# Kernel tuning notes

Measured on AMD Instinct MI355X. Metric: run time of the kernel, lower is better.

The kernel has to match this reference:

```python
import jax, jax.numpy as jnp
import numpy as np

N_COARSE = 64
N_FINE = 64  # n_fine_depth = 0
HIDDEN = 128
R = 16384


def setup_inputs() -> dict:
    key = jax.random.key(0)
    ks = jax.random.split(key, 8)
    origins = jax.random.normal(ks[0], (R, 3), dtype=jnp.float32)
    dirs = jax.random.normal(ks[1], (R, 3), dtype=jnp.float32)
    dirs = dirs / jnp.linalg.norm(dirs, axis=-1, keepdims=True)
    near = jnp.full((R, 1), 2.0, dtype=jnp.float32)
    far = jnp.full((R, 1), 6.0, dtype=jnp.float32)
    rays = jnp.concatenate([origins, dirs, near, far], axis=-1)  # [R, 8]
    u_coarse = jax.random.uniform(ks[2], (R, N_COARSE), dtype=jnp.float32)
    u_fine = jax.random.uniform(ks[3], (R, N_FINE), dtype=jnp.float32)
    u_jitter = jax.random.uniform(ks[4], (R, N_FINE), dtype=jnp.float32)
    W1 = jax.random.normal(ks[5], (3, HIDDEN), dtype=jnp.float32) * 0.5
    b1 = jnp.zeros((HIDDEN,), dtype=jnp.float32)
    W2 = jax.random.normal(ks[6], (HIDDEN, 4), dtype=jnp.float32) * 0.1
    b2 = jnp.zeros((4,), dtype=jnp.float32)
    return dict(rays=rays, u_coarse=u_coarse, u_fine=u_fine, u_jitter=u_jitter,
                W1=W1, b1=b1, W2=W2, b2=b2)


def _mlp(pts, W1, b1, W2, b2):
    # pts: [R, K, 3] -> [R, K, 4] (r, g, b, sigma)
    h = jax.nn.relu(pts @ W1 + b1)
    return h @ W2 + b2


def _composite(rays, z_sample, W1, b1, W2, b2):
    # z_sample: [R, K]; faithful to NeRFRenderer.composite
    deltas = jnp.concatenate(
        [z_sample[:, 1:] - z_sample[:, :-1], rays[:, 7:8] - z_sample[:, -1:]], axis=-1)
    pts = rays[:, None, :3] + z_sample[..., None] * rays[:, None, 3:6]  # [R, K, 3]
    out = _mlp(pts, W1, b1, W2, b2)
    rgbs = out[..., :3]
    sigmas = out[..., 3]
    alphas = 1.0 - jnp.exp(-deltas * jax.nn.relu(sigmas))
    alphas_shifted = jnp.concatenate(
        [jnp.ones_like(alphas[:, :1]), 1.0 - alphas + 1e-10], axis=-1)
    T = jnp.cumprod(alphas_shifted, axis=-1)
    weights = alphas * T[:, :-1]  # [R, K]
    rgb_final = jnp.sum(weights[..., None] * rgbs, axis=-2)  # [R, 3]
    depth_final = jnp.sum(weights * z_sample, axis=-1)       # [R]
    return weights, rgb_final, depth_final


def reference(rays, u_coarse, u_fine, u_jitter, W1, b1, W2, b2):
    near, far = rays[:, 6:7], rays[:, 7:8]
    # ---- coarse stratified sampling ----
    step = 1.0 / N_COARSE
    z_steps = jnp.linspace(0.0, 1.0 - step, N_COARSE, dtype=jnp.float32)[None, :] \
        + u_coarse * step
    z_coarse = near * (1.0 - z_steps) + far * z_steps  # [R, Kc] (lindisp=False)
    w_c, rgb_c, depth_c = _composite(rays, z_coarse, W1, b1, W2, b2)
    # ---- fine importance sampling (inverse CDF on detached coarse weights) ----
    w = jax.lax.stop_gradient(w_c) + 1e-5
    pdf = w / jnp.sum(w, axis=-1, keepdims=True)
    cdf = jnp.cumsum(pdf, axis=-1)
    cdf = jnp.concatenate([jnp.zeros_like(cdf[:, :1]), cdf], axis=-1)  # [R, Kc+1]
    inds = jax.vmap(lambda c, u: jnp.searchsorted(c, u, side='right'))(cdf, u_fine)
    inds = jnp.maximum(inds.astype(jnp.float32) - 1.0, 0.0)
    zf_steps = (inds + u_jitter) / N_COARSE
    z_fine = near * (1.0 - zf_steps) + far * zf_steps  # [R, Kf]
    z_all = jnp.sort(jnp.concatenate([z_coarse, z_fine], axis=-1), axis=-1)  # [R, Kc+Kf]
    w_f, rgb_f, depth_f = _composite(rays, z_all, W1, b1, W2, b2)
    # pack outputs: [R, 8] = [coarse rgb(3), coarse depth(1), fine rgb(3), fine depth(1)]
    return jnp.concatenate(
        [rgb_c, depth_c[:, None], rgb_f, depth_f[:, None]], axis=-1)
```

## Files before the change

### kernel.cpp

```cpp
#include <hip/hip_runtime.h>

#define HID 128

typedef _Float16 f16x8 __attribute__((ext_vector_type(8)));
typedef _Float16 f16x2 __attribute__((ext_vector_type(2)));
typedef float f32x4 __attribute__((ext_vector_type(4)));

union HV { f16x8 v; f16x2 h[4]; };
union F8 { float4 v[2]; float f[8]; };

template <int CTRL, int RM = 0xF, int BM = 0xF>
__device__ __forceinline__ float updf(float old, float src) {
    int o = __builtin_bit_cast(int, old);
    int s = __builtin_bit_cast(int, src);
    int r = __builtin_amdgcn_update_dpp(o, s, CTRL, RM, BM, false);
    return __builtin_bit_cast(float, r);
}

__device__ __forceinline__ float readlanef(float v, int l) {
    return __builtin_bit_cast(float, __builtin_amdgcn_readlane(__builtin_bit_cast(int, v), l));
}

__device__ __forceinline__ float dscan_add(float v) {
    v += updf<0x111>(0.0f, v);
    v += updf<0x112>(0.0f, v);
    v += updf<0x114>(0.0f, v);
    v += updf<0x118>(0.0f, v);
    v += updf<0x142, 0xA>(0.0f, v);
    v += updf<0x143, 0xC>(0.0f, v);
    return v;
}

__device__ __forceinline__ float dscan_mul(float v) {
    v *= updf<0x111>(1.0f, v);
    v *= updf<0x112>(1.0f, v);
    v *= updf<0x114>(1.0f, v);
    v *= updf<0x118>(1.0f, v);
    v *= updf<0x142, 0xA>(1.0f, v);
    v *= updf<0x143, 0xC>(1.0f, v);
    return v;
}

__device__ __forceinline__ float dexcl(float incl, float ident) {
    return updf<0x138>(ident, incl);
}
__device__ __forceinline__ float dnext(float v) {
    return updf<0x130>(0.0f, v);
}

template <int IMM>
__device__ __forceinline__ float swzf(float v) {
    return __builtin_bit_cast(float,
        __builtin_amdgcn_ds_swizzle(__builtin_bit_cast(int, v), IMM));
}

template <int M>
__device__ __forceinline__ float bx(float v) {
    if constexpr (M == 1)       return updf<0xB1>(v, v);
    else if constexpr (M == 2)  return updf<0x4E>(v, v);
    else if constexpr (M == 4)  return swzf<0x101F>(v);
    else if constexpr (M == 8)  return swzf<0x201F>(v);
    else if constexpr (M == 16) return swzf<0x401F>(v);
    else                        return __shfl_xor(v, 32, 64);
}

template <int M>
__device__ __forceinline__ float mstep(float x, int lane) {
    const float o = bx<M>(x);
    return ((lane & M) == 0) ? fminf(x, o) : fmaxf(x, o);
}

__device__ __forceinline__ f16x2 pk2(float a, float b) {
    return f16x2{ (_Float16)a, (_Float16)b };
}

__device__ __forceinline__ f32x4 mlp_tile(float zf,
                                          const HV P[4], const HV Q[4],
                                          const f16x8 w2t[4]) {
    const _Float16 zh = (_Float16)zf;
    const f16x2 zp = { zh, zh };
    const f16x2 zero2 = { (_Float16)0, (_Float16)0 };
    f32x4 C = { 0.0f, 0.0f, 0.0f, 0.0f };
#pragma unroll
    for (int c = 0; c < 4; ++c) {
        HV hb;
#pragma unroll
        for (int r = 0; r < 4; ++r) {
            f16x2 acc = Q[c].h[r] * zp + P[c].h[r];
            hb.h[r] = __builtin_elementwise_max(acc, zero2);
        }
        C = __builtin_amdgcn_mfma_f32_16x16x32_f16(w2t[c], hb.v, C, 0, 0, 0);
    }
    return C;
}

extern "C" __global__ void __launch_bounds__(256)
nerf_fused(const float* __restrict__ rays,
           const float* __restrict__ u_coarse,
           const float* __restrict__ u_fine,
           const float* __restrict__ u_jitter,
           const float* __restrict__ W1,
           const float* __restrict__ b1,
           const float* __restrict__ W2,
           const float* __restrict__ b2,
           float* __restrict__ out) {
    const int lane = threadIdx.x & 63;
    const int wv   = threadIdx.x >> 6;
    const int ray  = (blockIdx.x << 2) + wv;
    const int s16  = lane & 15;
    const int g    = lane >> 4;

    __shared__ float s_cdf[4][65];
    __shared__ float s_zc [4][64];
    __shared__ float s_za [4][128];

    const float* rp = rays + ray * 8;
    const float ox = rp[0], oy = rp[1], oz = rp[2];
    const float dx = rp[3], dy = rp[4], dz = rp[5];
    const float nearv = rp[6], farv = rp[7];

    HV P[4], Q[4];
#pragma unroll
    for (int c = 0; c < 4; ++c) {
        const int hid0 = 32 * c + 8 * g;
        F8 wa, wb, wc, bb;
        wa.v[0] = *(const float4*)(W1 + hid0);
        wa.v[1] = *(const float4*)(W1 + hid0 + 4);
        wb.v[0] = *(const float4*)(W1 + HID + hid0);
        wb.v[1] = *(const float4*)(W1 + HID + hid0 + 4);
        wc.v[0] = *(const float4*)(W1 + 2 * HID + hid0);
        wc.v[1] = *(const float4*)(W1 + 2 * HID + hid0 + 4);
        bb.v[0] = *(const float4*)(b1 + hid0);
        bb.v[1] = *(const float4*)(b1 + hid0 + 4);
        HV Pv, Qv;
#pragma unroll
        for (int r = 0; r < 4; ++r) {
            const float a0 = wa.f[2 * r], a1 = wa.f[2 * r + 1];
            const float e0 = wb.f[2 * r], e1 = wb.f[2 * r + 1];
            const float c0 = wc.f[2 * r], c1 = wc.f[2 * r + 1];
            const float f0 = bb.f[2 * r], f1 = bb.f[2 * r + 1];
            const float p0 = fmaf(ox, a0, fmaf(oy, e0, fmaf(oz, c0, f0)));
            const float p1 = fmaf(ox, a1, fmaf(oy, e1, fmaf(oz, c1, f1)));
            const float q0 = fmaf(dx, a0, fmaf(dy, e0, dz * c0));
            const float q1 = fmaf(dx, a1, fmaf(dy, e1, dz * c1));
            Pv.h[r] = pk2(p0, p1);
            Qv.h[r] = pk2(q0, q1);
        }
        P[c] = Pv; Q[c] = Qv;
    }

    f16x8 w2t[4];
#pragma unroll
    for (int c = 0; c < 4; ++c) {
        HV u;
#pragma unroll
        for (int r = 0; r < 4; ++r) {
            const int k0 = 32 * c + 8 * g + 2 * r;
            const float a0 = W2[k0 * 4 + (s16 & 3)];
            const float a1 = W2[(k0 + 1) * 4 + (s16 & 3)];
            u.h[r] = pk2(a0, a1);
        }
        w2t[c] = u.v;
    }
    const float b2s0 = b2[0], b2s1 = b2[1], b2s2 = b2[2], b2s3 = b2[3];

    const float uc = u_coarse[(ray << 6) + lane];
    const float zsv = ((float)lane + uc) * 0.015625f;
    const float zc = nearv * (1.0f - zsv) + farv * zsv;
    s_zc[wv][lane] = zc;

    f32x4 cv;
#pragma unroll
    for (int t = 0; t < 4; ++t) {
        const float ztv = s_zc[wv][t * 16 + s16];
        const f32x4 Ct = mlp_tile(ztv, P, Q, w2t);
        cv = (t == 0) ? Ct : ((g == t) ? Ct : cv);
    }
    cv[0] += b2s0; cv[1] += b2s1; cv[2] += b2s2; cv[3] += b2s3;

    {
        const float znext = dnext(zc);
        const float delta = (lane == 63) ? (farv - zc) : (znext - zc);
        const float alpha = 1.0f - __expf(-delta * fmaxf(cv[3], 0.0f));

        const float f  = 1.0f - alpha + 1e-10f;
        const float ip = dscan_mul(f);
        const float Te = dexcl(ip, 1.0f);
        const float w  = alpha * Te;

        const float rS = dscan_add(w * cv[0]);
        const float gS = dscan_add(w * cv[1]);
        const float bS = dscan_add(w * cv[2]);
        const float dS = dscan_add(w * zc);

        const float wp = w + 1e-5f;
        const float cs = dscan_add(wp);
        const float total = readlanef(cs, 63);
        if (lane == 0) s_cdf[wv][0] = 0.0f;
        s_cdf[wv][lane + 1] = cs / total;

        if (lane == 63) {
            float4* op = (float4*)(out + ray * 8);
            op[0] = make_float4(rS, gS, bS, dS);
        }
    }

    const float uf = u_fine[(ray << 6) + lane];
    const float uj = u_jitter[(ray << 6) + lane];

    int lo = 0, hi = 65;
#pragma unroll
    for (int it = 0; it < 7; ++it) {
        if (lo < hi) {
            int mid = (lo + hi) >> 1;
            if (s_cdf[wv][mid] <= uf) lo = mid + 1; else hi = mid;
        }
    }
    const float ind = fmaxf((float)lo - 1.0f, 0.0f);
    const float zfs = (ind + uj) * 0.015625f;
    const float zfv = nearv * (1.0f - zfs) + farv * zfs;

    float v = zfv;
#define BSTEP(K, J) { float o = bx<J>(v);                               \
                      bool asc = ((lane & K) != 0);                     \
                      bool low = ((lane & J) == 0);                     \
                      float mn = fminf(v, o), mx = fmaxf(v, o);         \
                      v = (asc == low) ? mn : mx; }
    BSTEP(2, 1)
    BSTEP(4, 2)  BSTEP(4, 1)
    BSTEP(8, 4)  BSTEP(8, 2)  BSTEP(8, 1)
    BSTEP(16, 8) BSTEP(16, 4) BSTEP(16, 2) BSTEP(16, 1)
    BSTEP(32, 16) BSTEP(32, 8) BSTEP(32, 4) BSTEP(32, 2) BSTEP(32, 1)
    BSTEP(64, 32) BSTEP(64, 16) BSTEP(64, 8) BSTEP(64, 4) BSTEP(64, 2) BSTEP(64, 1)
#undef BSTEP

    float zA = fminf(zc, v);
    float zB = fmaxf(zc, v);
    zA = mstep<32>(zA, lane); zB = mstep<32>(zB, lane);
    zA = mstep<16>(zA, lane); zB = mstep<16>(zB, lane);
    zA = mstep< 8>(zA, lane); zB = mstep< 8>(zB, lane);
    zA = mstep< 4>(zA, lane); zB = mstep< 4>(zB, lane);
    zA = mstep< 2>(zA, lane); zB = mstep< 2>(zB, lane);
    zA = mstep< 1>(zA, lane); zB = mstep< 1>(zB, lane);

    s_za[wv][lane]      = zA;
    s_za[wv][lane + 64] = zB;

    f32x4 vA;
#pragma unroll
    for (int t = 0; t < 4; ++t) {
        const float ztv = s_za[wv][t * 16 + s16];
        const f32x4 Ct = mlp_tile(ztv, P, Q, w2t);
        vA = (t == 0) ? Ct : ((g == t) ? Ct : vA);
    }
    f32x4 vB;
#pragma unroll
    for (int t = 0; t < 4; ++t) {
        const float ztv = s_za[wv][64 + t * 16 + s16];
        const f32x4 Ct = mlp_tile(ztv, P, Q, w2t);
        vB = (t == 0) ? Ct : ((g == t) ? Ct : vB);
    }
    vA[0] += b2s0; vA[1] += b2s1; vA[2] += b2s2; vA[3] += b2s3;
    vB[0] += b2s0; vB[1] += b2s1; vB[2] += b2s2; vB[3] += b2s3;

    {
        const float zA1 = dnext(zA);
        const float zB1 = dnext(zB);
        const float zB0 = readlanef(zB, 0);
        const float dA = (lane == 63) ? (zB0 - zA) : (zA1 - zA);
        const float dB = (lane == 63) ? (farv - zB) : (zB1 - zB);

        const float aA = 1.0f - __expf(-dA * fmaxf(vA[3], 0.0f));
        const float aB = 1.0f - __expf(-dB * fmaxf(vB[3], 0.0f));
        const float fA = 1.0f - aA + 1e-10f;
        const float fB = 1.0f - aB + 1e-10f;

        const float ipA = dscan_mul(fA);
        const float TA  = dexcl(ipA, 1.0f);
        const float wA  = aA * TA;

        const float Pall = readlanef(ipA, 63);
        const float ipB = dscan_mul(fB);
        const float TBp = dexcl(ipB, 1.0f);
        const float wB  = aB * Pall * TBp;

        const float rS = dscan_add(fmaf(wA, vA[0], wB * vB[0]));
        const float gS = dscan_add(fmaf(wA, vA[1], wB * vB[1]));
        const float bS = dscan_add(fmaf(wA, vA[2], wB * vB[2]));
        const float dS = dscan_add(fmaf(wA, zA, wB * zB));

        if (lane == 63) {
            float4* op = (float4*)(out + ray * 8);
            op[1] = make_float4(rS, gS, bS, dS);
        }
    }
}

extern "C" void kernel_launch(void* const* d_in, const int* in_sizes, int n_in,
                              void* d_out, int out_size, void* d_ws, size_t ws_size,
                              hipStream_t stream) {
    const float* rays = (const float*)d_in[0];
    const float* uc   = (const float*)d_in[1];
    const float* uf   = (const float*)d_in[2];
    const float* uj   = (const float*)d_in[3];
    const float* W1   = (const float*)d_in[4];
    const float* b1   = (const float*)d_in[5];
    const float* W2   = (const float*)d_in[6];
    const float* b2   = (const float*)d_in[7];
    float* o          = (float*)d_out;

    const int R = in_sizes[0] / 8;
    dim3 grid(R / 4), block(256);
    hipLaunchKernelGGL(nerf_fused, grid, block, 0, stream,
                       rays, uc, uf, uj, W1, b1, W2, b2, o);
}
```

Before: 118.2 us.

## Process two rays per wavefront to interleave independent dependency chains

Each wavefront now handles two rays instead of one, duplicating the per-ray state and interleaving the MLP tiles, DPP scans, binary search, bitonic sort and merge for both rays. The intent is to hide the latency of the MFMA, DPP and LDS chains through instruction-level parallelism, and to spread the W2 fragment setup and per-wave overhead across two rays. The grid is halved. Register pressure roughly doubles for the P/Q fragments and accumulators, which can lower occupancy or cause spills, and there are fewer waves in flight to hide latency.

```diff
diff --git a/kernel.cpp b/kernel.cpp
--- a/kernel.cpp
+++ b/kernel.cpp
@@ -106,20 +106,26 @@
            float* __restrict__ out) {
     const int lane = threadIdx.x & 63;
     const int wv   = threadIdx.x >> 6;
-    const int ray  = (blockIdx.x << 2) + wv;
+    const int wid  = (blockIdx.x << 2) + wv;
+    const int rayA = wid << 1;
+    const int rayB = rayA + 1;
     const int s16  = lane & 15;
     const int g    = lane >> 4;
 
-    __shared__ float s_cdf[4][65];
-    __shared__ float s_zc [4][64];
-    __shared__ float s_za [4][128];
-
-    const float* rp = rays + ray * 8;
-    const float ox = rp[0], oy = rp[1], oz = rp[2];
-    const float dx = rp[3], dy = rp[4], dz = rp[5];
-    const float nearv = rp[6], farv = rp[7];
-
-    HV P[4], Q[4];
+    __shared__ float s_cdf[4][2][65];
+    __shared__ float s_zc [4][2][64];
+    __shared__ float s_za [4][2][128];
+
+    const float* rpA = rays + rayA * 8;
+    const float* rpB = rays + rayB * 8;
+    const float oxA = rpA[0], oyA = rpA[1], ozA = rpA[2];
+    const float dxA = rpA[3], dyA = rpA[4], dzA = rpA[5];
+    const float nearA = rpA[6], farA = rpA[7];
+    const float oxB = rpB[0], oyB = rpB[1], ozB = rpB[2];
+    const float dxB = rpB[3], dyB = rpB[4], dzB = rpB[5];
+    const float nearB = rpB[6], farB = rpB[7];
+
+    HV PA[4], QA[4], PB[4], QB[4];
 #pragma unroll
     for (int c = 0; c < 4; ++c) {
         const int hid0 = 32 * c + 8 * g;
@@ -132,21 +138,23 @@
         wc.v[1] = *(const float4*)(W1 + 2 * HID + hid0 + 4);
         bb.v[0] = *(const float4*)(b1 + hid0);
         bb.v[1] = *(const float4*)(b1 + hid0 + 4);
-        HV Pv, Qv;
+        HV PvA, QvA, PvB, QvB;
 #pragma unroll
         for (int r = 0; r < 4; ++r) {
             const float a0 = wa.f[2 * r], a1 = wa.f[2 * r + 1];
             const float e0 = wb.f[2 * r], e1 = wb.f[2 * r + 1];
             const float c0 = wc.f[2 * r], c1 = wc.f[2 * r + 1];
             const float f0 = bb.f[2 * r], f1 = bb.f[2 * r + 1];
-            const float p0 = fmaf(ox, a0, fmaf(oy, e0, fmaf(oz, c0, f0)));
-            const float p1 = fmaf(ox, a1, fmaf(oy, e1, fmaf(oz, c1, f1)));
-            const float q0 = fmaf(dx, a0, fmaf(dy, e0, dz * c0));
-            const float q1 = fmaf(dx, a1, fmaf(dy, e1, dz * c1));
-            Pv.h[r] = pk2(p0, p1);
-            Qv.h[r] = pk2(q0, q1);
-        }
-        P[c] = Pv; Q[c] = Qv;
+            PvA.h[r] = pk2(fmaf(oxA, a0, fmaf(oyA, e0, fmaf(ozA, c0, f0))),
+                           fmaf(oxA, a1, fmaf(oyA, e1, fmaf(ozA, c1, f1))));
+            QvA.h[r] = pk2(fmaf(dxA, a0, fmaf(dyA, e0, dzA * c0)),
+                           fmaf(dxA, a1, fmaf(dyA, e1, dzA * c1)));
+            PvB.h[r] = pk2(fmaf(oxB, a0, fmaf(oyB, e0, fmaf(ozB, c0, f0))),
+                           fmaf(oxB, a1, fmaf(oyB, e1, fmaf(ozB, c1, f1))));
+            QvB.h[r] = pk2(fmaf(dxB, a0, fmaf(dyB, e0, dzB * c0)),
+                           fmaf(dxB, a1, fmaf(dyB, e1, dzB * c1)));
+        }
+        PA[c] = PvA; QA[c] = QvA; PB[c] = PvB; QB[c] = QvB;
     }
 
     f16x8 w2t[4];
@@ -156,76 +164,99 @@
 #pragma unroll
         for (int r = 0; r < 4; ++r) {
             const int k0 = 32 * c + 8 * g + 2 * r;
-            const float a0 = W2[k0 * 4 + (s16 & 3)];
-            const float a1 = W2[(k0 + 1) * 4 + (s16 & 3)];
-            u.h[r] = pk2(a0, a1);
+            u.h[r] = pk2(W2[k0 * 4 + (s16 & 3)], W2[(k0 + 1) * 4 + (s16 & 3)]);
         }
         w2t[c] = u.v;
     }
     const float b2s0 = b2[0], b2s1 = b2[1], b2s2 = b2[2], b2s3 = b2[3];
 
-    const float uc = u_coarse[(ray << 6) + lane];
-    const float zsv = ((float)lane + uc) * 0.015625f;
-    const float zc = nearv * (1.0f - zsv) + farv * zsv;
-    s_zc[wv][lane] = zc;
-
-    f32x4 cv;
+    const float ucA = u_coarse[(rayA << 6) + lane];
+    const float ucB = u_coarse[(rayB << 6) + lane];
+    const float zsA = ((float)lane + ucA) * 0.015625f;
+    const float zsB = ((float)lane + ucB) * 0.015625f;
+    const float zcA = nearA * (1.0f - zsA) + farA * zsA;
+    const float zcB = nearB * (1.0f - zsB) + farB * zsB;
+    s_zc[wv][0][lane] = zcA;
+    s_zc[wv][1][lane] = zcB;
+
+    f32x4 cvA, cvB;
 #pragma unroll
     for (int t = 0; t < 4; ++t) {
-        const float ztv = s_zc[wv][t * 16 + s16];
-        const f32x4 Ct = mlp_tile(ztv, P, Q, w2t);
-        cv = (t == 0) ? Ct : ((g == t) ? Ct : cv);
-    }
-    cv[0] += b2s0; cv[1] += b2s1; cv[2] += b2s2; cv[3] += b2s3;
+        const float ztA = s_zc[wv][0][t * 16 + s16];
+        const float ztB = s_zc[wv][1][t * 16 + s16];
+        const f32x4 CtA = mlp_tile(ztA, PA, QA, w2t);
+        const f32x4 CtB = mlp_tile(ztB, PB, QB, w2t);
+        cvA = (t == 0) ? CtA : ((g == t) ? CtA : cvA);
+        cvB = (t == 0) ? CtB : ((g == t) ? CtB : cvB);
+    }
+    cvA[0] += b2s0; cvA[1] += b2s1; cvA[2] += b2s2; cvA[3] += b2s3;
+    cvB[0] += b2s0; cvB[1] += b2s1; cvB[2] += b2s2; cvB[3] += b2s3;
 
     {
-        const float znext = dnext(zc);
-        const float delta = (lane == 63) ? (farv - zc) : (znext - zc);
-        const float alpha = 1.0f - __expf(-delta * fmaxf(cv[3], 0.0f));
-
-        const float f  = 1.0f - alpha + 1e-10f;
-        const float ip = dscan_mul(f);
-        const float Te = dexcl(ip, 1.0f);
-        const float w  = alpha * Te;
-
-        const float rS = dscan_add(w * cv[0]);
-        const float gS = dscan_add(w * cv[1]);
-        const float bS = dscan_add(w * cv[2]);
-        const float dS = dscan_add(w * zc);
-
-        const float wp = w + 1e-5f;
-        const float cs = dscan_add(wp);
-        const float total = readlanef(cs, 63);
-        if (lane == 0) s_cdf[wv][0] = 0.0f;
-        s_cdf[wv][lane + 1] = cs / total;
+        const float znA = dnext(zcA);
+        const float znB = dnext(zcB);
+        const float dltA = (lane == 63) ? (farA - zcA) : (znA - zcA);
+        const float dltB = (lane == 63) ? (farB - zcB) : (znB - zcB);
+        const float alA = 1.0f - __expf(-dltA * fmaxf(cvA[3], 0.0f));
+        const float alB = 1.0f - __expf(-dltB * fmaxf(cvB[3], 0.0f));
+
+        const float fA = 1.0f - alA + 1e-10f;
+        const float fB = 1.0f - alB + 1e-10f;
+        const float ipA = dscan_mul(fA);
+        const float ipB = dscan_mul(fB);
+        const float wA = alA * dexcl(ipA, 1.0f);
+        const float wB = alB * dexcl(ipB, 1.0f);
+
+        const float rSA = dscan_add(wA * cvA[0]);
+        const float rSB = dscan_add(wB * cvB[0]);
+        const float gSA = dscan_add(wA * cvA[1]);
+        const float gSB = dscan_add(wB * cvB[1]);
+        const float bSA = dscan_add(wA * cvA[2]);
+        const float bSB = dscan_add(wB * cvB[2]);
+        const float dSA = dscan_add(wA * zcA);
+        const float dSB = dscan_add(wB * zcB);
+
+        const float csA = dscan_add(wA + 1e-5f);
+        const float csB = dscan_add(wB + 1e-5f);
+        const float totA = readlanef(csA, 63);
+        const float totB = readlanef(csB, 63);
+        if (lane == 0) { s_cdf[wv][0][0] = 0.0f; s_cdf[wv][1][0] = 0.0f; }
+        s_cdf[wv][0][lane + 1] = csA / totA;
+        s_cdf[wv][1][lane + 1] = csB / totB;
 
         if (lane == 63) {
-            float4* op = (float4*)(out + ray * 8);
-            op[0] = make_float4(rS, gS, bS, dS);
-        }
-    }
-
-    const float uf = u_fine[(ray << 6) + lane];
-    const float uj = u_jitter[(ray << 6) + lane];
-
-    int lo = 0, hi = 65;
+            *(float4*)(out + rayA * 8) = make_float4(rSA, gSA, bSA, dSA);
+            *(float4*)(out + rayB * 8) = make_float4(rSB, gSB, bSB, dSB);
+        }
+    }
+
+    const float ufA = u_fine[(rayA << 6) + lane];
+    const float ufB = u_fine[(rayB << 6) + lane];
+    const float ujA = u_jitter[(rayA << 6) + lane];
+    const float ujB = u_jitter[(rayB << 6) + lane];
+
+    int loA = 0, hiA = 65, loB = 0, hiB = 65;
 #pragma unroll
     for (int it = 0; it < 7; ++it) {
-        if (lo < hi) {
-            int mid = (lo + hi) >> 1;
-            if (s_cdf[wv][mid] <= uf) lo = mid + 1; else hi = mid;
-        }
-    }
-    const float ind = fmaxf((float)lo - 1.0f, 0.0f);
-    const float zfs = (ind + uj) * 0.015625f;
-    const float zfv = nearv * (1.0f - zfs) + farv * zfs;
-
-    float v = zfv;
-#define BSTEP(K, J) { float o = bx<J>(v);                               \
-                      bool asc = ((lane & K) != 0);                     \
-                      bool low = ((lane & J) == 0);                     \
-                      float mn = fminf(v, o), mx = fmaxf(v, o);         \
-                      v = (asc == low) ? mn : mx; }
+        if (loA < hiA) {
+            int mid = (loA + hiA) >> 1;
+            if (s_cdf[wv][0][mid] <= ufA) loA = mid + 1; else hiA = mid;
+        }
+        if (loB < hiB) {
+            int mid = (loB + hiB) >> 1;
+            if (s_cdf[wv][1][mid] <= ufB) loB = mid + 1; else hiB = mid;
+        }
+    }
+    const float zfsA = (fmaxf((float)loA - 1.0f, 0.0f) + ujA) * 0.015625f;
+    const float zfsB = (fmaxf((float)loB - 1.0f, 0.0f) + ujB) * 0.015625f;
+    float vA = nearA * (1.0f - zfsA) + farA * zfsA;
+    float vB = nearB * (1.0f - zfsB) + farB * zfsB;
+
+#define BSTEP(K, J) { float oA = bx<J>(vA); float oB = bx<J>(vB);          \
+                      bool asc = ((lane & K) != 0);                        \
+                      bool low = ((lane & J) == 0);                        \
+                      vA = (asc == low) ? fminf(vA, oA) : fmaxf(vA, oA);   \
+                      vB = (asc == low) ? fminf(vB, oB) : fmaxf(vB, oB); }
     BSTEP(2, 1)
     BSTEP(4, 2)  BSTEP(4, 1)
     BSTEP(8, 4)  BSTEP(8, 2)  BSTEP(8, 1)
@@ -234,64 +265,93 @@
     BSTEP(64, 32) BSTEP(64, 16) BSTEP(64, 8) BSTEP(64, 4) BSTEP(64, 2) BSTEP(64, 1)
 #undef BSTEP
 
-    float zA = fminf(zc, v);
-    float zB = fmaxf(zc, v);
-    zA = mstep<32>(zA, lane); zB = mstep<32>(zB, lane);
-    zA = mstep<16>(zA, lane); zB = mstep<16>(zB, lane);
-    zA = mstep< 8>(zA, lane); zB = mstep< 8>(zB, lane);
-    zA = mstep< 4>(zA, lane); zB = mstep< 4>(zB, lane);
-    zA = mstep< 2>(zA, lane); zB = mstep< 2>(zB, lane);
-    zA = mstep< 1>(zA, lane); zB = mstep< 1>(zB, lane);
-
-    s_za[wv][lane]      = zA;
-    s_za[wv][lane + 64] = zB;
-
-    f32x4 vA;
+    float zAA = fminf(zcA, vA), zAB = fmaxf(zcA, vA);
+    float zBA = fminf(zcB, vB), zBB = fmaxf(zcB, vB);
+    zAA = mstep<32>(zAA, lane); zAB = mstep<32>(zAB, lane);
+    zBA = mstep<32>(zBA, lane); zBB = mstep<32>(zBB, lane);
+    zAA = mstep<16>(zAA, lane); zAB = mstep<16>(zAB, lane);
+    zBA = mstep<16>(zBA, lane); zBB = mstep<16>(zBB, lane);
+    zAA = mstep< 8>(zAA, lane); zAB = mstep< 8>(zAB, lane);
+    zBA = mstep< 8>(zBA, lane); zBB = mstep< 8>(zBB, lane);
+    zAA = mstep< 4>(zAA, lane); zAB = mstep< 4>(zAB, lane);
+    zBA = mstep< 4>(zBA, lane); zBB = mstep< 4>(zBB, lane);
+    zAA = mstep< 2>(zAA, lane); zAB = mstep< 2>(zAB, lane);
+    zBA = mstep< 2>(zBA, lane); zBB = mstep< 2>(zBB, lane);
+    zAA = mstep< 1>(zAA, lane); zAB = mstep< 1>(zAB, lane);
+    zBA = mstep< 1>(zBA, lane); zBB = mstep< 1>(zBB, lane);
+
+    s_za[wv][0][lane]      = zAA;
+    s_za[wv][0][lane + 64] = zAB;
+    s_za[wv][1][lane]      = zBA;
+    s_za[wv][1][lane + 64] = zBB;
+
+    f32x4 vAA, vAB, vBA, vBB;
 #pragma unroll
     for (int t = 0; t < 4; ++t) {
-        const float ztv = s_za[wv][t * 16 + s16];
-        const f32x4 Ct = mlp_tile(ztv, P, Q, w2t);
-        vA = (t == 0) ? Ct : ((g == t) ? Ct : vA);
-    }
-    f32x4 vB;
+        const float z1 = s_za[wv][0][t * 16 + s16];
+        const float z2 = s_za[wv][1][t * 16 + s16];
+        const f32x4 C1 = mlp_tile(z1, PA, QA, w2t);
+        const f32x4 C2 = mlp_tile(z2, PB, QB, w2t);
+        vAA = (t == 0) ? C1 : ((g == t) ? C1 : vAA);
+        vBA = (t == 0) ? C2 : ((g == t) ? C2 : vBA);
+    }
 #pragma unroll
     for (int t = 0; t < 4; ++t) {
-        const float ztv = s_za[wv][64 + t * 16 + s16];
-        const f32x4 Ct = mlp_tile(ztv, P, Q, w2t);
-        vB = (t == 0) ? Ct : ((g == t) ? Ct : vB);
-    }
-    vA[0] += b2s0; vA[1] += b2s1; vA[2] += b2s2; vA[3] += b2s3;
-    vB[0] += b2s0; vB[1] += b2s1; vB[2] += b2s2; vB[3] += b2s3;
+        const float z1 = s_za[wv][0][64 + t * 16 + s16];
+        const float z2 = s_za[wv][1][64 + t * 16 + s16];
+        const f32x4 C1 = mlp_tile(z1, PA, QA, w2t);
+        const f32x4 C2 = mlp_tile(z2, PB, QB, w2t);
+        vAB = (t == 0) ? C1 : ((g == t) ? C1 : vAB);
+        vBB = (t == 0) ? C2 : ((g == t) ? C2 : vBB);
+    }
+    vAA[0] += b2s0; vAA[1] += b2s1; vAA[2] += b2s2; vAA[3] += b2s3;
+    vAB[0] += b2s0; vAB[1] += b2s1; vAB[2] += b2s2; vAB[3] += b2s3;
+    vBA[0] += b2s0; vBA[1] += b2s1; vBA[2] += b2s2; vBA[3] += b2s3;
+    vBB[0] += b2s0; vBB[1] += b2s1; vBB[2] += b2s2; vBB[3] += b2s3;
 
     {
-        const float zA1 = dnext(zA);
-        const float zB1 = dnext(zB);
-        const float zB0 = readlanef(zB, 0);
-        const float dA = (lane == 63) ? (zB0 - zA) : (zA1 - zA);
-        const float dB = (lane == 63) ? (farv - zB) : (zB1 - zB);
-
-        const float aA = 1.0f - __expf(-dA * fmaxf(vA[3], 0.0f));
-        const float aB = 1.0f - __expf(-dB * fmaxf(vB[3], 0.0f));
-        const float fA = 1.0f - aA + 1e-10f;
-        const float fB = 1.0f - aB + 1e-10f;
-
-        const float ipA = dscan_mul(fA);
-        const float TA  = dexcl(ipA, 1.0f);
-        const float wA  = aA * TA;
-
-        const float Pall = readlanef(ipA, 63);
-        const float ipB = dscan_mul(fB);
-        const float TBp = dexcl(ipB, 1.0f);
-        const float wB  = aB * Pall * TBp;
-
-        const float rS = dscan_add(fmaf(wA, vA[0], wB * vB[0]));
-        const float gS = dscan_add(fmaf(wA, vA[1], wB * vB[1]));
-        const float bS = dscan_add(fmaf(wA, vA[2], wB * vB[2]));
-        const float dS = dscan_add(fmaf(wA, zA, wB * zB));
+        const float zA1 = dnext(zAA), zA2 = dnext(zAB);
+        const float zB1 = dnext(zBA), zB2 = dnext(zBB);
+        const float zA0 = readlanef(zAB, 0);
+        const float zB0 = readlanef(zBB, 0);
+        const float dAA = (lane == 63) ? (zA0 - zAA) : (zA1 - zAA);
+        const float dAB = (lane == 63) ? (farA - zAB) : (zA2 - zAB);
+        const float dBA = (lane == 63) ? (zB0 - zBA) : (zB1 - zBA);
+        const float dBB = (lane == 63) ? (farB - zBB) : (zB2 - zBB);
+
+        const float aAA = 1.0f - __expf(-dAA * fmaxf(vAA[3], 0.0f));
+        const float aAB = 1.0f - __expf(-dAB * fmaxf(vAB[3], 0.0f));
+        const float aBA = 1.0f - __expf(-dBA * fmaxf(vBA[3], 0.0f));
+        const float aBB = 1.0f - __expf(-dBB * fmaxf(vBB[3], 0.0f));
+        const float fAA = 1.0f - aAA + 1e-10f;
+        const float fAB = 1.0f - aAB + 1e-10f;
+        const float fBA = 1.0f - aBA + 1e-10f;
+        const float fBB = 1.0f - aBB + 1e-10f;
+
+        const float ipAA = dscan_mul(fAA);
+        const float ipBA = dscan_mul(fBA);
+        const float wAA = aAA * dexcl(ipAA, 1.0f);
+        const float wBA = aBA * dexcl(ipBA, 1.0f);
+
+        const float PallA = readlanef(ipAA, 63);
+        const float PallB = readlanef(ipBA, 63);
+        const float ipAB = dscan_mul(fAB);
+        const float ipBB = dscan_mul(fBB);
+        const float wAB = aAB * PallA * dexcl(ipAB, 1.0f);
+        const float wBB = aBB * PallB * dexcl(ipBB, 1.0f);
+
+        const float rSA = dscan_add(fmaf(wAA, vAA[0], wAB * vAB[0]));
+        const float rSB = dscan_add(fmaf(wBA, vBA[0], wBB * vBB[0]));
+        const float gSA = dscan_add(fmaf(wAA, vAA[1], wAB * vAB[1]));
+        const float gSB = dscan_add(fmaf(wBA, vBA[1], wBB * vBB[1]));
+        const float bSA = dscan_add(fmaf(wAA, vAA[2], wAB * vAB[2]));
+        const float bSB = dscan_add(fmaf(wBA, vBA[2], wBB * vBB[2]));
+        const float dSA = dscan_add(fmaf(wAA, zAA, wAB * zAB));
+        const float dSB = dscan_add(fmaf(wBA, zBA, wBB * zBB));
 
         if (lane == 63) {
-            float4* op = (float4*)(out + ray * 8);
-            op[1] = make_float4(rS, gS, bS, dS);
+            *(float4*)(out + rayA * 8 + 4) = make_float4(rSA, gSA, bSA, dSA);
+            *(float4*)(out + rayB * 8 + 4) = make_float4(rSB, gSB, bSB, dSB);
         }
     }
 }
@@ -310,7 +370,7 @@
     float* o          = (float*)d_out;
 
     const int R = in_sizes[0] / 8;
-    dim3 grid(R / 4), block(256);
+    dim3 grid(R / 8), block(256);
     hipLaunchKernelGGL(nerf_fused, grid, block, 0, stream,
                        rays, uc, uf, uj, W1, b1, W2, b2, o);
 }
```

Result: no change. 116.4 us (-1.5%).
